# Performance work log

Hardware: AMD Instinct MI355X
Metric: run time of the kernel (lower is better)

The kernel has to match this reference:

```python
import jax, jax.numpy as jnp
import numpy as np

# AlphaFold-style Invariant Point Attention (the StructureModule's core op)
N, SD, PD, C, H, PQ, PV = 768, 384, 128, 16, 12, 4, 8
W_C = (2.0 / (9.0 * PQ)) ** 0.5   # point-distance weight
W_L = (1.0 / 3.0) ** 0.5          # logit balancing weight
INV_SQRT_C = C ** -0.5


def setup_inputs() -> dict:
    key = jax.random.key(0)
    ks = jax.random.split(key, 11)
    single_rep = jax.random.normal(ks[0], (N, SD), jnp.float32)
    pair_rep = jax.random.normal(ks[1], (N, N, PD), jnp.float32)
    # random rigid frames: proper orthonormal rotations via QR + translations
    M = jax.random.normal(ks[2], (N, 3, 3), jnp.float32)
    frames_R, _ = jnp.linalg.qr(M)
    frames_t = jax.random.normal(ks[3], (N, 3), jnp.float32) * 10.0
    s = 0.02
    W_qkv = jax.random.normal(ks[4], (SD, 3 * H * C), jnp.float32) * s
    W_b = jax.random.normal(ks[5], (PD, H), jnp.float32) * s
    W_qkp = jax.random.normal(ks[6], (SD, 2 * H * PQ * 3), jnp.float32) * s
    W_vp = jax.random.normal(ks[7], (SD, H * PV * 3), jnp.float32) * s
    gamma = jnp.zeros((H,), jnp.float32)
    W_out = jax.random.normal(ks[8], (H * (PD + C + 3 * PV + PV), SD), jnp.float32) * s
    b_out = jnp.zeros((SD,), jnp.float32)
    return dict(single_rep=single_rep, pair_rep=pair_rep, frames_R=frames_R,
                frames_t=frames_t, W_qkv=W_qkv, W_b=W_b, W_qkp=W_qkp,
                W_vp=W_vp, gamma=gamma, W_out=W_out, b_out=b_out)


def reference(single_rep, pair_rep, frames_R, frames_t,
              W_qkv, W_b, W_qkp, W_vp, gamma, W_out, b_out):
    n = single_rep.shape[0]
    # scalar q/k/v: [n, C, H] (module views as (proj_dim, n_heads))
    q, k, v = [x.reshape(n, C, H) for x in jnp.split(single_rep @ W_qkv, 3, axis=-1)]
    b = jnp.einsum('ijd,dh->ijh', pair_rep, W_b)             # pair bias [n,n,H]
    qp, kp = [x.reshape(n, PQ, 3, H) for x in jnp.split(single_rep @ W_qkp, 2, axis=-1)]
    vp = (single_rep @ W_vp).reshape(n, PV, 3, H)

    def to_global(p):  # apply frame T_i = (R_i, t_i) to local points
        return jnp.einsum('nxy,npyh->npxh', frames_R, p) + frames_t[:, None, :, None]

    qg, kg, vg = to_global(qp), to_global(kp), to_global(vp)

    # squared distances sum_p ||T_i q_p - T_j k_p||^2 without [n,n,PQ,3,H] temp
    sq = jnp.sum(qg * qg, axis=(1, 2))                       # [n,H]
    sk = jnp.sum(kg * kg, axis=(1, 2))                       # [n,H]
    cross = jnp.einsum('ipxh,jpxh->ijh', qg, kg)             # [n,n,H]
    dist2 = sq[:, None, :] + sk[None, :, :] - 2.0 * cross

    head_w = jax.nn.softplus(gamma)                          # per-head gamma
    logits = W_L * (INV_SQRT_C * jnp.einsum('ich,jch->ijh', q, k)
                    + b - 0.5 * W_C * head_w * dist2)
    attn = jax.nn.softmax(logits, axis=1)                    # softmax over j

    o_pair = jnp.einsum('ijh,ijd->ihd', attn, pair_rep)      # [n,H,PD]
    o = jnp.einsum('ijh,jch->ihc', attn, v)                  # [n,H,C]
    og = jnp.einsum('ijh,jpxh->ipxh', attn, vg)              # [n,PV,3,H]
    # back to local frame: R_i^T (og - t_i)
    ol = jnp.einsum('nyx,npyh->npxh', frames_R, og - frames_t[:, None, :, None])
    onorm = jnp.sqrt(jnp.sum(ol * ol, axis=2) + 1e-8)        # [n,PV,H]

    feats = jnp.concatenate([
        o_pair.reshape(n, -1),
        o.reshape(n, -1),
        jnp.moveaxis(ol, -1, 1).reshape(n, -1),
        jnp.moveaxis(onorm, -1, 1).reshape(n, -1)], axis=-1)  # [n, H*(PD+C+3PV+PV)]
    return feats @ W_out + b_out
```

## Files before the change

### kernel.cpp

```cpp
#include <hip/hip_runtime.h>
#include <hip/hip_bf16.h>

typedef float v4f __attribute__((ext_vector_type(4)));
typedef short bf8 __attribute__((ext_vector_type(8)));
typedef unsigned short u16;

constexpr float W_C_ = 0.23570226039551584f;
constexpr float W_L_ = 0.5773502691896258f;

__device__ __forceinline__ u16 f2bf(float f) {
  unsigned u = __float_as_uint(f);
  return (u16)((u + 0x7FFFu + ((u >> 16) & 1u)) >> 16);
}
__device__ __forceinline__ float bf2f(u16 h) {
  return __uint_as_float(((unsigned)h) << 16);
}
__device__ __forceinline__ float dot4(v4f a, v4f b) {
  return a.x * b.x + a.y * b.y + a.z * b.z + a.w * b.w;
}

__global__ __launch_bounds__(256) void convert_bf(const float* __restrict__ src,
                                                  u16* __restrict__ dst, int n8) {
  int idx = blockIdx.x * 256 + threadIdx.x;
  if (idx < n8) {
    v4f a = ((const v4f*)src)[idx * 2];
    v4f b = ((const v4f*)src)[idx * 2 + 1];
    bf8 o;
    o[0] = (short)f2bf(a.x); o[1] = (short)f2bf(a.y);
    o[2] = (short)f2bf(a.z); o[3] = (short)f2bf(a.w);
    o[4] = (short)f2bf(b.x); o[5] = (short)f2bf(b.y);
    o[6] = (short)f2bf(b.z); o[7] = (short)f2bf(b.w);
    ((bf8*)dst)[idx] = o;
  }
}

__global__ __launch_bounds__(256) void wfrag_k(const float* __restrict__ W,
                                               u16* __restrict__ frag,
                                               int K, int N, float scale) {
  __shared__ float Ws[32 * 384];
  const int ks = blockIdx.x, k0 = ks * 32, t = threadIdx.x;
  const int NTfull = (N + 15) >> 4;
  for (int n0 = 0; n0 < N; n0 += 384) {
    int PN = N - n0; if (PN > 384) PN = 384;
    __syncthreads();
    for (int idx = t; idx < 32 * PN; idx += 256) {
      int r = idx / PN, c = idx - r * PN;
      Ws[r * PN + c] = W[(size_t)(k0 + r) * N + n0 + c];
    }
    __syncthreads();
    int NTp = (PN + 15) >> 4;
    for (int c = t; c < NTp * 64; c += 256) {
      int nt = c >> 6, l = c & 63;
      int col = nt * 16 + (l & 15);
      bf8 o;
#pragma unroll
      for (int e = 0; e < 8; e++) {
        int rr = (l >> 4) * 8 + e;
        float f = (col < PN) ? Ws[rr * PN + col] * scale : 0.f;
        o[e] = (short)f2bf(f);
      }
      ((bf8*)frag)[((size_t)ks * NTfull + (n0 >> 4) + nt) * 64 + l] = o;
    }
  }
}

__global__ __launch_bounds__(256) void mfma_gemm(
    const u16* __restrict__ Abf, const u16* __restrict__ Bfrag,
    const float* __restrict__ bias, float* __restrict__ C,
    int M, int N, int K, int ldc) {
  __shared__ u16 As[64 * 32];
  const int t = threadIdx.x, w = t >> 6, l = t & 63;
  const int bi = blockIdx.y * 64, nt0 = blockIdx.x * 2;
  const int NT = N >> 4, KS = K >> 5;
  v4f acc0 = {0.f, 0.f, 0.f, 0.f}, acc1 = {0.f, 0.f, 0.f, 0.f};
  const int srow = t >> 2, sc = t & 3;
  const int wslot = (sc ^ (srow & 3)) * 8;
  const bf8* Bf = (const bf8*)Bfrag;

  bf8 areg = *(const bf8*)(Abf + (size_t)(bi + srow) * K + sc * 8);
  bf8 b0 = Bf[(size_t)(0 * NT + nt0) * 64 + l];
  bf8 b1 = Bf[(size_t)(0 * NT + nt0 + 1) * 64 + l];
  const int rdoff = (w * 16 + (l & 15)) * 32 + (((l >> 4) ^ (l & 3)) * 8);
  for (int ks = 0; ks < KS; ks++) {
    *(bf8*)&As[srow * 32 + wslot] = areg;
    bf8 an, bn0, bn1;
    if (ks + 1 < KS) {
      an = *(const bf8*)(Abf + (size_t)(bi + srow) * K + (ks + 1) * 32 + sc * 8);
      bn0 = Bf[(size_t)((ks + 1) * NT + nt0) * 64 + l];
      bn1 = Bf[(size_t)((ks + 1) * NT + nt0 + 1) * 64 + l];
    }
    __syncthreads();
    bf8 af = *(const bf8*)&As[rdoff];
    acc0 = __builtin_amdgcn_mfma_f32_16x16x32_bf16(af, b0, acc0, 0, 0, 0);
    acc1 = __builtin_amdgcn_mfma_f32_16x16x32_bf16(af, b1, acc1, 0, 0, 0);
    __syncthreads();
    areg = an; b0 = bn0; b1 = bn1;
  }
  int col0 = nt0 * 16 + (l & 15), col1 = col0 + 16;
  float bb0 = bias ? bias[col0] : 0.f;
  float bb1 = bias ? bias[col1] : 0.f;
#pragma unroll
  for (int r = 0; r < 4; r++) {
    int row = bi + w * 16 + (l >> 4) * 4 + r;
    C[(size_t)row * ldc + col0] = acc0[r] + bb0;
    C[(size_t)row * ldc + col1] = acc1[r] + bb1;
  }
}

__global__ __launch_bounds__(256) void prep_kernel(
    const float* __restrict__ projQKV, const float* __restrict__ projQKP,
    const float* __restrict__ projVP, const float* __restrict__ fR,
    const float* __restrict__ ft,
    float* __restrict__ qbuf, float* __restrict__ kbuf, float* __restrict__ v2buf,
    float* __restrict__ qgbuf, float* __restrict__ kgbuf,
    float* __restrict__ sqbuf, float* __restrict__ skbuf) {
  const int n = blockIdx.x, t = threadIdx.x;
  __shared__ float R[9], tt[3];
  __shared__ float qgL[144], kgL[144];
  if (t < 9) R[t] = fR[n * 9 + t];
  if (t < 3) tt[t] = ft[n * 3 + t];
  __syncthreads();
  const float* rQKV = projQKV + (size_t)n * 576;
  const float* rQKP = projQKP + (size_t)n * 288;
  const float* rVP = projVP + (size_t)n * 288;
  if (t < 192) {
    int h = t >> 4, c = t & 15;
    qbuf[(size_t)n * 192 + t] = rQKV[c * 12 + h];
    kbuf[(size_t)n * 192 + t] = rQKV[192 + c * 12 + h];
    v2buf[(size_t)n * 480 + h * 40 + c] = rQKV[384 + c * 12 + h];
  }
  if (t < 144) {
    int e = t / 12, h = t % 12;
    int p = e / 3, x = e % 3;
    float aq = tt[x], ak = tt[x];
#pragma unroll
    for (int y = 0; y < 3; y++) {
      float r = R[x * 3 + y];
      aq += r * rQKP[p * 36 + y * 12 + h];
      ak += r * rQKP[144 + p * 36 + y * 12 + h];
    }
    qgL[h * 12 + e] = aq;
    kgL[h * 12 + e] = ak;
    qgbuf[(size_t)n * 144 + h * 12 + e] = aq;
    kgbuf[(size_t)n * 144 + h * 12 + e] = ak;
  }
  for (int idx = t; idx < 288; idx += 256) {
    int e = idx / 12, h = idx % 12;
    int p = e / 3, x = e % 3;
    float a = tt[x];
#pragma unroll
    for (int y = 0; y < 3; y++) a += R[x * 3 + y] * rVP[p * 36 + y * 12 + h];
    v2buf[(size_t)n * 480 + h * 40 + 16 + e] = a;
  }
  __syncthreads();
  if (t < 12) {
    float s = 0.f;
#pragma unroll
    for (int e = 0; e < 12; e++) { float v = qgL[t * 12 + e]; s += v * v; }
    sqbuf[n * 12 + t] = s;
  } else if (t < 24) {
    int h = t - 12;
    float s = 0.f;
#pragma unroll
    for (int e = 0; e < 12; e++) { float v = kgL[h * 12 + e]; s += v * v; }
    skbuf[n * 12 + h] = s;
  }
}

__global__ __launch_bounds__(256) void biaslogit_k(
    const float* __restrict__ pair, const u16* __restrict__ WbFrag,
    const float* __restrict__ gamma,
    const float* __restrict__ qbuf, const float* __restrict__ kbuf,
    const float* __restrict__ qgbuf, const float* __restrict__ kgbuf,
    const float* __restrict__ sqbuf, const float* __restrict__ skbuf,
    u16* __restrict__ pair_bf, float* __restrict__ logits) {
  const int jt = blockIdx.x, i = blockIdx.y;
  const int t = threadIdx.x, w = t >> 6, l = t & 63;
  __shared__ u16 pS[64 * 128];
  __shared__ float lgL[64 * 15];
  __shared__ float qL[192], qgL[144], c1L[12], c2L[12];

  if (t < 192) qL[t] = qbuf[(size_t)i * 192 + t];
  if (t < 144) qgL[t] = qgbuf[(size_t)i * 144 + t];
  if (t < 12) {
    float g = gamma[t];
    float hw = fmaxf(g, 0.f) + log1pf(expf(-fabsf(g)));
    c1L[t] = W_L_ * W_C_ * hw;
    c2L[t] = -0.5f * c1L[t] * sqbuf[i * 12 + t];
  }
  bf8 wb[4];
  const bf8* Wf = (const bf8*)WbFrag;
#pragma unroll
  for (int ks = 0; ks < 4; ks++) wb[ks] = Wf[ks * 64 + l];

  const float* pg = pair + ((size_t)i * 768 + jt * 64) * 128;
  u16* pbg = pair_bf + ((size_t)i * 768 + jt * 64) * 128;
#pragma unroll
  for (int it = 0; it < 4; it++) {
    int idx = t + 256 * it;
    int j = idx >> 4, c = idx & 15;
    v4f x0 = *(const v4f*)(pg + j * 128 + c * 8);
    v4f x1 = *(const v4f*)(pg + j * 128 + c * 8 + 4);
    bf8 pk;
    pk[0] = (short)f2bf(x0.x); pk[1] = (short)f2bf(x0.y);
    pk[2] = (short)f2bf(x0.z); pk[3] = (short)f2bf(x0.w);
    pk[4] = (short)f2bf(x1.x); pk[5] = (short)f2bf(x1.y);
    pk[6] = (short)f2bf(x1.z); pk[7] = (short)f2bf(x1.w);
    *(bf8*)&pS[j * 128 + ((c ^ (j & 15)) * 8)] = pk;
    *(bf8*)(pbg + j * 128 + c * 8) = pk;
  }
  __syncthreads();

  {
    v4f acc = {0.f, 0.f, 0.f, 0.f};
#pragma unroll
    for (int ks = 0; ks < 4; ks++) {
      int slot = (ks * 4 + (l >> 4)) ^ (l & 15);
      bf8 af = *(const bf8*)&pS[(w * 16 + (l & 15)) * 128 + slot * 8];
      acc = __builtin_amdgcn_mfma_f32_16x16x32_bf16(af, wb[ks], acc, 0, 0, 0);
    }
    int h = l & 15;
    if (h < 12) {
#pragma unroll
      for (int r = 0; r < 4; r++)
        lgL[(w * 16 + (l >> 4) * 4 + r) * 15 + h] = acc[r];
    }
  }
  __syncthreads();

  {
    const int j = t >> 2, hg = t & 3;
    const int jg = jt * 64 + j;
#pragma unroll
    for (int hh = 0; hh < 3; hh++) {
      int h = hg * 3 + hh;
      const v4f* kk = (const v4f*)(kbuf + (size_t)jg * 192 + h * 16);
      const v4f* qq = (const v4f*)&qL[h * 16];
      float qk = dot4(kk[0], qq[0]) + dot4(kk[1], qq[1]) +
                 dot4(kk[2], qq[2]) + dot4(kk[3], qq[3]);
      const v4f* kg = (const v4f*)(kgbuf + (size_t)jg * 144 + h * 12);
      const v4f* qg = (const v4f*)&qgL[h * 12];
      float cr = dot4(kg[0], qg[0]) + dot4(kg[1], qg[1]) + dot4(kg[2], qg[2]);
      float sk = skbuf[(size_t)jg * 12 + h];
      lgL[j * 15 + h] += 0.25f * W_L_ * qk + c1L[h] * (cr - 0.5f * sk) + c2L[h];
    }
  }
  __syncthreads();

#pragma unroll
  for (int s = 0; s < 3; s++) {
    int o = t + 256 * s;
    int h = o >> 6, j = o & 63;
    logits[((size_t)i * 12 + h) * 768 + jt * 64 + j] = lgL[j * 15 + h];
  }
}

__global__ __launch_bounds__(256) void softmax_bf(const float* __restrict__ L,
                                                  u16* __restrict__ attn) {
  const int row = blockIdx.x * 4 + (threadIdx.x >> 6);
  const int lane = threadIdx.x & 63;
  const v4f* p = (const v4f*)(L + (size_t)row * 768);
  v4f a0 = p[lane], a1 = p[lane + 64], a2 = p[lane + 128];
  float m0 = fmaxf(fmaxf(a0.x, a0.y), fmaxf(a0.z, a0.w));
  float m1 = fmaxf(fmaxf(a1.x, a1.y), fmaxf(a1.z, a1.w));
  float m2 = fmaxf(fmaxf(a2.x, a2.y), fmaxf(a2.z, a2.w));
  float m = fmaxf(m0, fmaxf(m1, m2));
#pragma unroll
  for (int s = 32; s >= 1; s >>= 1) m = fmaxf(m, __shfl_xor(m, s));
  a0.x = __expf(a0.x - m); a0.y = __expf(a0.y - m);
  a0.z = __expf(a0.z - m); a0.w = __expf(a0.w - m);
  a1.x = __expf(a1.x - m); a1.y = __expf(a1.y - m);
  a1.z = __expf(a1.z - m); a1.w = __expf(a1.w - m);
  a2.x = __expf(a2.x - m); a2.y = __expf(a2.y - m);
  a2.z = __expf(a2.z - m); a2.w = __expf(a2.w - m);
  float s = a0.x + a0.y + a0.z + a0.w + a1.x + a1.y + a1.z + a1.w +
            a2.x + a2.y + a2.z + a2.w;
#pragma unroll
  for (int q = 32; q >= 1; q >>= 1) s += __shfl_xor(s, q);
  float inv = 1.f / s;
  a0 *= inv; a1 *= inv; a2 *= inv;
  u16* arow = attn + (size_t)row * 768;
  uint2 pk;
  pk.x = (unsigned)f2bf(a0.x) | ((unsigned)f2bf(a0.y) << 16);
  pk.y = (unsigned)f2bf(a0.z) | ((unsigned)f2bf(a0.w) << 16);
  *(uint2*)&arow[lane * 4] = pk;
  pk.x = (unsigned)f2bf(a1.x) | ((unsigned)f2bf(a1.y) << 16);
  pk.y = (unsigned)f2bf(a1.z) | ((unsigned)f2bf(a1.w) << 16);
  *(uint2*)&arow[256 + lane * 4] = pk;
  pk.x = (unsigned)f2bf(a2.x) | ((unsigned)f2bf(a2.y) << 16);
  pk.y = (unsigned)f2bf(a2.z) | ((unsigned)f2bf(a2.w) << 16);
  *(uint2*)&arow[512 + lane * 4] = pk;
}

__global__ __launch_bounds__(256) void opair_k(
    const u16* __restrict__ pair_bf, const u16* __restrict__ attn,
    u16* __restrict__ feats_bf) {
  const int i = blockIdx.x, t = threadIdx.x;
  const int w = t >> 6, l = t & 63;
  const int dq = l & 31, hh = l >> 5;
  __shared__ float smemf[6160];
  u16* pS = (u16*)smemf;
  float* ALf = smemf + 4096;
  float* red = smemf;

  v4f acc[6];
#pragma unroll
  for (int k = 0; k < 6; k++) acc[k] = (v4f){0.f, 0.f, 0.f, 0.f};

  bf8 pr[4];
  bf8 areg;
  {
    const u16* pg = pair_bf + (size_t)i * 768 * 128;
#pragma unroll
    for (int it = 0; it < 4; it++) {
      int idx = t + 256 * it;
      pr[it] = *(const bf8*)(pg + (idx >> 4) * 128 + (idx & 15) * 8);
    }
    if (t < 96)
      areg = *(const bf8*)(attn + ((size_t)i * 12 + (t >> 3)) * 768 + (t & 7) * 8);
  }
  for (int jt = 0; jt < 12; jt++) {
#pragma unroll
    for (int it = 0; it < 4; it++) {
      int idx = t + 256 * it;
      int j = idx >> 4, c = idx & 15;
      *(bf8*)&pS[j * 128 + ((c ^ (j & 15)) * 8)] = pr[it];
    }
    if (t < 96) {
      int hA = t >> 3, c = t & 7;
#pragma unroll
      for (int e = 0; e < 8; e++) ALf[hA * 68 + c * 8 + e] = bf2f((u16)areg[e]);
    }
    if (jt < 11) {
      const u16* pg = pair_bf + ((size_t)i * 768 + (jt + 1) * 64) * 128;
#pragma unroll
      for (int it = 0; it < 4; it++) {
        int idx = t + 256 * it;
        pr[it] = *(const bf8*)(pg + (idx >> 4) * 128 + (idx & 15) * 8);
      }
      if (t < 96)
        areg = *(const bf8*)(attn + ((size_t)i * 12 + (t >> 3)) * 768 +
                             (jt + 1) * 64 + (t & 7) * 8);
    }
    __syncthreads();
#pragma unroll
    for (int jj16 = 0; jj16 < 16; jj16++) {
      int jj = w * 16 + jj16;
      const u16* pv4 = &pS[jj * 128 + (((dq >> 1) ^ (jj & 15)) * 8) + (dq & 1) * 4];
      v4f pv;
      pv.x = bf2f(pv4[0]); pv.y = bf2f(pv4[1]);
      pv.z = bf2f(pv4[2]); pv.w = bf2f(pv4[3]);
      float a0 = ALf[(hh * 6 + 0) * 68 + jj];
      float a1 = ALf[(hh * 6 + 1) * 68 + jj];
      float a2 = ALf[(hh * 6 + 2) * 68 + jj];
      float a3 = ALf[(hh * 6 + 3) * 68 + jj];
      float a4 = ALf[(hh * 6 + 4) * 68 + jj];
      float a5 = ALf[(hh * 6 + 5) * 68 + jj];
      acc[0] += pv * a0; acc[1] += pv * a1; acc[2] += pv * a2;
      acc[3] += pv * a3; acc[4] += pv * a4; acc[5] += pv * a5;
    }
    __syncthreads();
  }
#pragma unroll
  for (int k = 0; k < 6; k++)
    *(v4f*)&red[(w * 12 + hh * 6 + k) * 128 + dq * 4] = acc[k];
  __syncthreads();
  const size_t fb = (size_t)i * 2112;
#pragma unroll
  for (int s = 0; s < 6; s++) {
    int o = t + 256 * s;
    int ho = o >> 7, dd = o & 127;
    float v = red[ho * 128 + dd] + red[(12 + ho) * 128 + dd] +
              red[(24 + ho) * 128 + dd] + red[(36 + ho) * 128 + dd];
    feats_bf[fb + o] = f2bf(v);
  }
}

__global__ __launch_bounds__(256) void ov_k(
    const u16* __restrict__ attn, const float* __restrict__ v2buf,
    float* __restrict__ O2) {
  const int i0 = blockIdx.x * 64, h = blockIdx.y, t = threadIdx.x;
  __shared__ float AL[64][65];
  __shared__ float VL[64][48];
  const int il = t & 63, eb = (t >> 6) * 12;
  v4f acc0 = {0.f, 0.f, 0.f, 0.f}, acc1 = {0.f, 0.f, 0.f, 0.f},
      acc2 = {0.f, 0.f, 0.f, 0.f};
  for (int jt = 0; jt < 12; ++jt) {
    const int j0 = jt * 64;
#pragma unroll
    for (int q = 0; q < 2; q++) {
      int idx = t + 256 * q;
      int ii = idx >> 3, c = idx & 7;
      bf8 av = *(const bf8*)(attn + ((size_t)(i0 + ii) * 12 + h) * 768 + j0 + c * 8);
#pragma unroll
      for (int e = 0; e < 8; e++) AL[ii][c * 8 + e] = bf2f((u16)av[e]);
    }
#pragma unroll
    for (int q = 0; q < 3; q++) {
      int idx = t + q * 256;
      if (idx < 640) {
        int jj = idx / 10, e4 = idx % 10;
        *(v4f*)&VL[jj][e4 * 4] =
            *(const v4f*)(v2buf + (size_t)(j0 + jj) * 480 + h * 40 + e4 * 4);
      }
    }
    __syncthreads();
#pragma unroll 4
    for (int jj = 0; jj < 64; ++jj) {
      float a = AL[il][jj];
      v4f v0 = *(const v4f*)&VL[jj][eb];
      v4f v1 = *(const v4f*)&VL[jj][eb + 4];
      v4f v2 = *(const v4f*)&VL[jj][eb + 8];
      acc0 += v0 * a;
      acc1 += v1 * a;
      acc2 += v2 * a;
    }
    __syncthreads();
  }
  float* orow = O2 + ((size_t)(i0 + il) * 12 + h) * 40;
#pragma unroll
  for (int s = 0; s < 12; ++s) {
    int e = eb + s;
    if (e < 40) {
      float v = (s < 4) ? ((float*)&acc0)[s]
                        : (s < 8) ? ((float*)&acc1)[s - 4] : ((float*)&acc2)[s - 8];
      orow[e] = v;
    }
  }
}

__global__ __launch_bounds__(256) void finalize_k(
    const float* __restrict__ O2, const float* __restrict__ fR,
    const float* __restrict__ ft, u16* __restrict__ feats_bf) {
  const int i = blockIdx.x, t = threadIdx.x;
  __shared__ float RL[9], ttL[3];
  if (t < 9) RL[t] = fR[i * 9 + t];
  if (t < 3) ttL[t] = ft[i * 3 + t];
  __syncthreads();
  const float* orow = O2 + (size_t)i * 480;
  const size_t fb = (size_t)i * 2112;
  if (t < 192) {
    int h = t >> 4, c = t & 15;
    feats_bf[fb + 1536 + h * 16 + c] = f2bf(orow[h * 40 + c]);
  }
  if (t < 96) {
    int h = t >> 3, p = t & 7;
    float og0 = orow[h * 40 + 16 + p * 3 + 0] - ttL[0];
    float og1 = orow[h * 40 + 16 + p * 3 + 1] - ttL[1];
    float og2 = orow[h * 40 + 16 + p * 3 + 2] - ttL[2];
    float o0 = RL[0] * og0 + RL[3] * og1 + RL[6] * og2;
    float o1 = RL[1] * og0 + RL[4] * og1 + RL[7] * og2;
    float o2 = RL[2] * og0 + RL[5] * og1 + RL[8] * og2;
    feats_bf[fb + 1728 + h * 24 + p * 3 + 0] = f2bf(o0);
    feats_bf[fb + 1728 + h * 24 + p * 3 + 1] = f2bf(o1);
    feats_bf[fb + 1728 + h * 24 + p * 3 + 2] = f2bf(o2);
    feats_bf[fb + 2016 + h * 8 + p] = f2bf(sqrtf(o0 * o0 + o1 * o1 + o2 * o2 + 1e-8f));
  }
}

extern "C" void kernel_launch(void* const* d_in, const int* in_sizes, int n_in,
                              void* d_out, int out_size, void* d_ws, size_t ws_size,
                              hipStream_t stream) {
  const float* single = (const float*)d_in[0];
  const float* pair = (const float*)d_in[1];
  const float* fR = (const float*)d_in[2];
  const float* ft = (const float*)d_in[3];
  const float* W_qkv = (const float*)d_in[4];
  const float* W_b = (const float*)d_in[5];
  const float* W_qkp = (const float*)d_in[6];
  const float* W_vp = (const float*)d_in[7];
  const float* gamma = (const float*)d_in[8];
  const float* W_out = (const float*)d_in[9];
  const float* b_out = (const float*)d_in[10];
  float* out = (float*)d_out;

  float* ws = (float*)d_ws;
  float* projQKV = ws;
  float* projQKP = ws + 442368;
  float* projVP  = ws + 663552;
  float* qbuf    = ws + 884736;
  float* kbuf    = ws + 1032192;
  float* v2buf   = ws + 1179648;
  float* qgbuf   = ws + 1548288;
  float* kgbuf   = ws + 1658880;
  float* sqbuf   = ws + 1769472;
  float* skbuf   = ws + 1778688;
  float* logits  = ws + 1787904;
  float* O2      = ws + 8865792;
  u16* ub        = (u16*)(ws + 9234432);
  u16* single_bf = ub;
  u16* WqkvFrag  = ub + 294912;
  u16* WqkpFrag  = ub + 516096;
  u16* WvpFrag   = ub + 626688;
  u16* WbFrag    = ub + 737280;
  u16* WoutFrag  = ub + 739328;
  u16* attn      = ub + 1550336;
  u16* feats_bf  = ub + 8628224;
  u16* pair_bf   = ub + 10250240;

  convert_bf<<<144, 256, 0, stream>>>(single, single_bf, 36864);
  wfrag_k<<<12, 256, 0, stream>>>(W_qkv, WqkvFrag, 384, 576, 1.f);
  wfrag_k<<<12, 256, 0, stream>>>(W_qkp, WqkpFrag, 384, 288, 1.f);
  wfrag_k<<<12, 256, 0, stream>>>(W_vp, WvpFrag, 384, 288, 1.f);
  wfrag_k<<<4, 256, 0, stream>>>(W_b, WbFrag, 128, 12, W_L_);
  wfrag_k<<<66, 256, 0, stream>>>(W_out, WoutFrag, 2112, 384, 1.f);
  mfma_gemm<<<dim3(18, 12), 256, 0, stream>>>(single_bf, WqkvFrag, nullptr,
                                              projQKV, 768, 576, 384, 576);
  mfma_gemm<<<dim3(9, 12), 256, 0, stream>>>(single_bf, WqkpFrag, nullptr,
                                             projQKP, 768, 288, 384, 288);
  mfma_gemm<<<dim3(9, 12), 256, 0, stream>>>(single_bf, WvpFrag, nullptr,
                                             projVP, 768, 288, 384, 288);
  prep_kernel<<<768, 256, 0, stream>>>(projQKV, projQKP, projVP, fR, ft,
                                       qbuf, kbuf, v2buf, qgbuf, kgbuf, sqbuf, skbuf);
  biaslogit_k<<<dim3(12, 768), 256, 0, stream>>>(pair, WbFrag, gamma, qbuf, kbuf,
                                                 qgbuf, kgbuf, sqbuf, skbuf,
                                                 pair_bf, logits);
  softmax_bf<<<2304, 256, 0, stream>>>(logits, attn);
  opair_k<<<768, 256, 0, stream>>>(pair_bf, attn, feats_bf);
  ov_k<<<dim3(12, 12), 256, 0, stream>>>(attn, v2buf, O2);
  finalize_k<<<768, 256, 0, stream>>>(O2, fR, ft, feats_bf);
  mfma_gemm<<<dim3(12, 12), 256, 0, stream>>>(feats_bf, WoutFrag, b_out,
                                              out, 768, 384, 2112, 384);
}
```

Before: 353.0 us.

## Merge prep launches, fuse projection GEMMs, fold finalize into ov kernel

Combines the single-rep bf16 conversion and all weight-fragment packing into one launch, and merges the three projection GEMMs into a single GEMM over a concatenated weight. The ov kernel now performs the frame back-transform and norm and writes feats directly, which removes the finalize kernel and its O2 round trip. In biaslogit, the pair_bf global write moves after the logits store and reads back from LDS. The aim is fewer launches and less intermediate traffic, at the cost of lower parallelism in the finalize step (only 144 blocks).

```diff
diff --git a/kernel.cpp b/kernel.cpp
--- a/kernel.cpp
+++ b/kernel.cpp
@@ -19,27 +19,10 @@
   return a.x * b.x + a.y * b.y + a.z * b.z + a.w * b.w;
 }
 
-__global__ __launch_bounds__(256) void convert_bf(const float* __restrict__ src,
-                                                  u16* __restrict__ dst, int n8) {
-  int idx = blockIdx.x * 256 + threadIdx.x;
-  if (idx < n8) {
-    v4f a = ((const v4f*)src)[idx * 2];
-    v4f b = ((const v4f*)src)[idx * 2 + 1];
-    bf8 o;
-    o[0] = (short)f2bf(a.x); o[1] = (short)f2bf(a.y);
-    o[2] = (short)f2bf(a.z); o[3] = (short)f2bf(a.w);
-    o[4] = (short)f2bf(b.x); o[5] = (short)f2bf(b.y);
-    o[6] = (short)f2bf(b.z); o[7] = (short)f2bf(b.w);
-    ((bf8*)dst)[idx] = o;
-  }
-}
-
-__global__ __launch_bounds__(256) void wfrag_k(const float* __restrict__ W,
-                                               u16* __restrict__ frag,
-                                               int K, int N, float scale) {
-  __shared__ float Ws[32 * 384];
-  const int ks = blockIdx.x, k0 = ks * 32, t = threadIdx.x;
-  const int NTfull = (N + 15) >> 4;
+__device__ void wfrag_dev(const float* __restrict__ W, u16* __restrict__ frag,
+                          int K, int N, float scale, int ks, int ntBase,
+                          int NTtotal, float* Ws, int t) {
+  const int k0 = ks * 32;
   for (int n0 = 0; n0 < N; n0 += 384) {
     int PN = N - n0; if (PN > 384) PN = 384;
     __syncthreads();
@@ -59,8 +42,40 @@
         float f = (col < PN) ? Ws[rr * PN + col] * scale : 0.f;
         o[e] = (short)f2bf(f);
       }
-      ((bf8*)frag)[((size_t)ks * NTfull + (n0 >> 4) + nt) * 64 + l] = o;
-    }
+      ((bf8*)frag)[((size_t)ks * NTtotal + ntBase + (n0 >> 4) + nt) * 64 + l] = o;
+    }
+  }
+}
+
+__global__ __launch_bounds__(256) void wfrag_all(
+    const float* __restrict__ single, u16* __restrict__ single_bf,
+    const float* __restrict__ W_qkv, const float* __restrict__ W_qkp,
+    const float* __restrict__ W_vp, const float* __restrict__ W_b,
+    const float* __restrict__ W_out,
+    u16* __restrict__ WallFrag, u16* __restrict__ WbFrag,
+    u16* __restrict__ WoutFrag) {
+  __shared__ float Ws[32 * 384];
+  const int b = blockIdx.x, t = threadIdx.x;
+  if (b < 144) {
+    int idx = b * 256 + t;
+    v4f a = ((const v4f*)single)[idx * 2];
+    v4f c = ((const v4f*)single)[idx * 2 + 1];
+    bf8 o;
+    o[0] = (short)f2bf(a.x); o[1] = (short)f2bf(a.y);
+    o[2] = (short)f2bf(a.z); o[3] = (short)f2bf(a.w);
+    o[4] = (short)f2bf(c.x); o[5] = (short)f2bf(c.y);
+    o[6] = (short)f2bf(c.z); o[7] = (short)f2bf(c.w);
+    ((bf8*)single_bf)[idx] = o;
+  } else if (b < 156) {
+    wfrag_dev(W_qkv, WallFrag, 384, 576, 1.f, b - 144, 0, 72, Ws, t);
+  } else if (b < 168) {
+    wfrag_dev(W_qkp, WallFrag, 384, 288, 1.f, b - 156, 36, 72, Ws, t);
+  } else if (b < 180) {
+    wfrag_dev(W_vp, WallFrag, 384, 288, 1.f, b - 168, 54, 72, Ws, t);
+  } else if (b < 184) {
+    wfrag_dev(W_b, WbFrag, 128, 12, W_L_, b - 180, 0, 1, Ws, t);
+  } else {
+    wfrag_dev(W_out, WoutFrag, 2112, 384, 1.f, b - 184, 0, 24, Ws, t);
   }
 }
 
@@ -108,8 +123,7 @@
 }
 
 __global__ __launch_bounds__(256) void prep_kernel(
-    const float* __restrict__ projQKV, const float* __restrict__ projQKP,
-    const float* __restrict__ projVP, const float* __restrict__ fR,
+    const float* __restrict__ projAll, const float* __restrict__ fR,
     const float* __restrict__ ft,
     float* __restrict__ qbuf, float* __restrict__ kbuf, float* __restrict__ v2buf,
     float* __restrict__ qgbuf, float* __restrict__ kgbuf,
@@ -120,9 +134,9 @@
   if (t < 9) R[t] = fR[n * 9 + t];
   if (t < 3) tt[t] = ft[n * 3 + t];
   __syncthreads();
-  const float* rQKV = projQKV + (size_t)n * 576;
-  const float* rQKP = projQKP + (size_t)n * 288;
-  const float* rVP = projVP + (size_t)n * 288;
+  const float* rQKV = projAll + (size_t)n * 1152;
+  const float* rQKP = rQKV + 576;
+  const float* rVP = rQKV + 864;
   if (t < 192) {
     int h = t >> 4, c = t & 15;
     qbuf[(size_t)n * 192 + t] = rQKV[c * 12 + h];
@@ -194,7 +208,6 @@
   for (int ks = 0; ks < 4; ks++) wb[ks] = Wf[ks * 64 + l];
 
   const float* pg = pair + ((size_t)i * 768 + jt * 64) * 128;
-  u16* pbg = pair_bf + ((size_t)i * 768 + jt * 64) * 128;
 #pragma unroll
   for (int it = 0; it < 4; it++) {
     int idx = t + 256 * it;
@@ -207,7 +220,6 @@
     pk[4] = (short)f2bf(x1.x); pk[5] = (short)f2bf(x1.y);
     pk[6] = (short)f2bf(x1.z); pk[7] = (short)f2bf(x1.w);
     *(bf8*)&pS[j * 128 + ((c ^ (j & 15)) * 8)] = pk;
-    *(bf8*)(pbg + j * 128 + c * 8) = pk;
   }
   __syncthreads();
 
@@ -252,6 +264,15 @@
     int o = t + 256 * s;
     int h = o >> 6, j = o & 63;
     logits[((size_t)i * 12 + h) * 768 + jt * 64 + j] = lgL[j * 15 + h];
+  }
+
+  u16* pbg = pair_bf + ((size_t)i * 768 + jt * 64) * 128;
+#pragma unroll
+  for (int it = 0; it < 4; it++) {
+    int idx = t + 256 * it;
+    int j = idx >> 4, c = idx & 15;
+    bf8 pk = *(const bf8*)&pS[j * 128 + ((c ^ (j & 15)) * 8)];
+    *(bf8*)(pbg + j * 128 + c * 8) = pk;
   }
 }
 
@@ -376,9 +397,10 @@
   }
 }
 
-__global__ __launch_bounds__(256) void ov_k(
+__global__ __launch_bounds__(256) void ovfin_k(
     const u16* __restrict__ attn, const float* __restrict__ v2buf,
-    float* __restrict__ O2) {
+    const float* __restrict__ fR, const float* __restrict__ ft,
+    u16* __restrict__ feats_bf) {
   const int i0 = blockIdx.x * 64, h = blockIdx.y, t = threadIdx.x;
   __shared__ float AL[64][65];
   __shared__ float VL[64][48];
@@ -417,44 +439,51 @@
     }
     __syncthreads();
   }
-  float* orow = O2 + ((size_t)(i0 + il) * 12 + h) * 40;
+  float* OL = &AL[0][0];
 #pragma unroll
   for (int s = 0; s < 12; ++s) {
     int e = eb + s;
     if (e < 40) {
       float v = (s < 4) ? ((float*)&acc0)[s]
                         : (s < 8) ? ((float*)&acc1)[s - 4] : ((float*)&acc2)[s - 8];
-      orow[e] = v;
-    }
-  }
-}
-
-__global__ __launch_bounds__(256) void finalize_k(
-    const float* __restrict__ O2, const float* __restrict__ fR,
-    const float* __restrict__ ft, u16* __restrict__ feats_bf) {
-  const int i = blockIdx.x, t = threadIdx.x;
-  __shared__ float RL[9], ttL[3];
-  if (t < 9) RL[t] = fR[i * 9 + t];
-  if (t < 3) ttL[t] = ft[i * 3 + t];
-  __syncthreads();
-  const float* orow = O2 + (size_t)i * 480;
-  const size_t fb = (size_t)i * 2112;
-  if (t < 192) {
-    int h = t >> 4, c = t & 15;
-    feats_bf[fb + 1536 + h * 16 + c] = f2bf(orow[h * 40 + c]);
-  }
-  if (t < 96) {
-    int h = t >> 3, p = t & 7;
-    float og0 = orow[h * 40 + 16 + p * 3 + 0] - ttL[0];
-    float og1 = orow[h * 40 + 16 + p * 3 + 1] - ttL[1];
-    float og2 = orow[h * 40 + 16 + p * 3 + 2] - ttL[2];
-    float o0 = RL[0] * og0 + RL[3] * og1 + RL[6] * og2;
-    float o1 = RL[1] * og0 + RL[4] * og1 + RL[7] * og2;
-    float o2 = RL[2] * og0 + RL[5] * og1 + RL[8] * og2;
-    feats_bf[fb + 1728 + h * 24 + p * 3 + 0] = f2bf(o0);
-    feats_bf[fb + 1728 + h * 24 + p * 3 + 1] = f2bf(o1);
-    feats_bf[fb + 1728 + h * 24 + p * 3 + 2] = f2bf(o2);
-    feats_bf[fb + 2016 + h * 8 + p] = f2bf(sqrtf(o0 * o0 + o1 * o1 + o2 * o2 + 1e-8f));
+      OL[il * 44 + e] = v;
+    }
+  }
+  __syncthreads();
+  {
+    const int ii = t >> 2, sub = t & 3;
+    const int ig = i0 + ii;
+    const float* orow = &OL[ii * 44];
+    const size_t fb = (size_t)ig * 2112;
+    if (sub == 0) {
+#pragma unroll
+      for (int c = 0; c < 16; c++)
+        feats_bf[fb + 1536 + h * 16 + c] = f2bf(orow[c]);
+    } else {
+      float R[9], tt[3];
+#pragma unroll
+      for (int k = 0; k < 9; k++) R[k] = fR[ig * 9 + k];
+#pragma unroll
+      for (int k = 0; k < 3; k++) tt[k] = ft[ig * 3 + k];
+      int p0 = (sub - 1) * 3, pn = (sub == 3) ? 2 : 3;
+#pragma unroll
+      for (int pp = 0; pp < 3; pp++) {
+        if (pp < pn) {
+          int p = p0 + pp;
+          float og0 = orow[16 + p * 3 + 0] - tt[0];
+          float og1 = orow[16 + p * 3 + 1] - tt[1];
+          float og2 = orow[16 + p * 3 + 2] - tt[2];
+          float o0 = R[0] * og0 + R[3] * og1 + R[6] * og2;
+          float o1 = R[1] * og0 + R[4] * og1 + R[7] * og2;
+          float o2 = R[2] * og0 + R[5] * og1 + R[8] * og2;
+          feats_bf[fb + 1728 + h * 24 + p * 3 + 0] = f2bf(o0);
+          feats_bf[fb + 1728 + h * 24 + p * 3 + 1] = f2bf(o1);
+          feats_bf[fb + 1728 + h * 24 + p * 3 + 2] = f2bf(o2);
+          feats_bf[fb + 2016 + h * 8 + p] =
+              f2bf(sqrtf(o0 * o0 + o1 * o1 + o2 * o2 + 1e-8f));
+        }
+      }
+    }
   }
 }
 
@@ -475,9 +504,7 @@
   float* out = (float*)d_out;
 
   float* ws = (float*)d_ws;
-  float* projQKV = ws;
-  float* projQKP = ws + 442368;
-  float* projVP  = ws + 663552;
+  float* projAll = ws;
   float* qbuf    = ws + 884736;
   float* kbuf    = ws + 1032192;
   float* v2buf   = ws + 1179648;
@@ -486,39 +513,27 @@
   float* sqbuf   = ws + 1769472;
   float* skbuf   = ws + 1778688;
   float* logits  = ws + 1787904;
-  float* O2      = ws + 8865792;
-  u16* ub        = (u16*)(ws + 9234432);
+  u16* ub        = (u16*)(ws + 8865792);
   u16* single_bf = ub;
-  u16* WqkvFrag  = ub + 294912;
-  u16* WqkpFrag  = ub + 516096;
-  u16* WvpFrag   = ub + 626688;
+  u16* WallFrag  = ub + 294912;
   u16* WbFrag    = ub + 737280;
   u16* WoutFrag  = ub + 739328;
   u16* attn      = ub + 1550336;
   u16* feats_bf  = ub + 8628224;
   u16* pair_bf   = ub + 10250240;
 
-  convert_bf<<<144, 256, 0, stream>>>(single, single_bf, 36864);
-  wfrag_k<<<12, 256, 0, stream>>>(W_qkv, WqkvFrag, 384, 576, 1.f);
-  wfrag_k<<<12, 256, 0, stream>>>(W_qkp, WqkpFrag, 384, 288, 1.f);
-  wfrag_k<<<12, 256, 0, stream>>>(W_vp, WvpFrag, 384, 288, 1.f);
-  wfrag_k<<<4, 256, 0, stream>>>(W_b, WbFrag, 128, 12, W_L_);
-  wfrag_k<<<66, 256, 0, stream>>>(W_out, WoutFrag, 2112, 384, 1.f);
-  mfma_gemm<<<dim3(18, 12), 256, 0, stream>>>(single_bf, WqkvFrag, nullptr,
-                                              projQKV, 768, 576, 384, 576);
-  mfma_gemm<<<dim3(9, 12), 256, 0, stream>>>(single_bf, WqkpFrag, nullptr,
-                                             projQKP, 768, 288, 384, 288);
-  mfma_gemm<<<dim3(9, 12), 256, 0, stream>>>(single_bf, WvpFrag, nullptr,
-                                             projVP, 768, 288, 384, 288);
-  prep_kernel<<<768, 256, 0, stream>>>(projQKV, projQKP, projVP, fR, ft,
-                                       qbuf, kbuf, v2buf, qgbuf, kgbuf, sqbuf, skbuf);
+  wfrag_all<<<250, 256, 0, stream>>>(single, single_bf, W_qkv, W_qkp, W_vp,
+                                     W_b, W_out, WallFrag, WbFrag, WoutFrag);
+  mfma_gemm<<<dim3(36, 12), 256, 0, stream>>>(single_bf, WallFrag, nullptr,
+                                              projAll, 768, 1152, 384, 1152);
+  prep_kernel<<<768, 256, 0, stream>>>(projAll, fR, ft, qbuf, kbuf, v2buf,
+                                       qgbuf, kgbuf, sqbuf, skbuf);
   biaslogit_k<<<dim3(12, 768), 256, 0, stream>>>(pair, WbFrag, gamma, qbuf, kbuf,
                                                  qgbuf, kgbuf, sqbuf, skbuf,
                                                  pair_bf, logits);
   softmax_bf<<<2304, 256, 0, stream>>>(logits, attn);
   opair_k<<<768, 256, 0, stream>>>(pair_bf, attn, feats_bf);
-  ov_k<<<dim3(12, 12), 256, 0, stream>>>(attn, v2buf, O2);
-  finalize_k<<<768, 256, 0, stream>>>(O2, fR, ft, feats_bf);
+  ovfin_k<<<dim3(12, 12), 256, 0, stream>>>(attn, v2buf, fR, ft, feats_bf);
   mfma_gemm<<<dim3(12, 12), 256, 0, stream>>>(feats_bf, WoutFrag, b_out,
                                               out, 768, 384, 2112, 384);
 }
```

New measurement: 296.9 us. 15.9% less time.
